# Kernel tuning notes

Hardware: AMD Instinct MI355X
Metric: run time of the kernel (lower is better)

The kernel has to match this reference:

```python
import jax, jax.numpy as jnp
import numpy as np

EPS = 1e-8
NEG_INF = -9e15  # matches torch masked_fill value


def setup_inputs() -> dict:
    key = jax.random.key(0)
    k1, k2 = jax.random.split(key)
    B, D = 4096, 512
    p1 = jax.random.normal(k1, (B, D), dtype=jnp.float32)
    p2 = jax.random.normal(k2, (B, D), dtype=jnp.float32)
    return {"p1": p1, "p2": p2}


def reference(p1, p2):
    # NT-Xent / InfoNCE loss as in SimCLR_MODEL.contrastive_loss (temperature = 1).
    z = jnp.concatenate([p1, p2], axis=0)              # [N, D], N = 2B
    # cosine similarity == GEMM of L2-normalized rows (torch eps clamp = 1e-8)
    zn = z / jnp.maximum(jnp.linalg.norm(z, axis=-1, keepdims=True), EPS)
    sim = zn @ zn.T                                     # [N, N]
    N = sim.shape[0]
    idx = jnp.arange(N)
    sim = sim.at[idx, idx].set(NEG_INF)                 # mask self-similarity
    # positive pair of row i is row (i + N/2) mod N (eye rolled by N/2)
    pos = sim[idx, (idx + N // 2) % N]                  # [N]
    nll = -pos + jax.nn.logsumexp(sim, axis=-1)
    return jnp.mean(nll)
```

## Files before the change

### kernel.cpp

```cpp
#include <hip/hip_runtime.h>
#include <hip/hip_bf16.h>
#include <math.h>

#define N_TOT 8192
#define HALF_N 4096
#define D_DIM 512
#define BM 128
#define BK 64
#define NKIT (D_DIM / BK)
#define NTILES 2080

#define WAIT_VM4 0xF74
#define WAIT_VM0 0xF70

typedef float f32x4_t __attribute__((ext_vector_type(4)));
typedef long long i64x2 __attribute__((ext_vector_type(2)));

typedef __attribute__((address_space(1))) unsigned int g_u32;
typedef __attribute__((address_space(3))) unsigned int l_u32;

__global__ __launch_bounds__(256) void k_normalize(
    const float* __restrict__ p1, const float* __restrict__ p2,
    unsigned char* __restrict__ zf8, float* __restrict__ rowsum,
    float* __restrict__ out)
{
    const int w = threadIdx.x >> 6;
    const int lane = threadIdx.x & 63;
    const int row = blockIdx.x * 4 + w;

    if (threadIdx.x < 4) rowsum[blockIdx.x * 4 + threadIdx.x] = 0.0f;
    if (blockIdx.x == 0 && threadIdx.x == 0) out[0] = 0.0f;

    const float* src = (row < HALF_N) ? p1 + (size_t)row * D_DIM
                                      : p2 + (size_t)(row - HALF_N) * D_DIM;
    float4 a = *(const float4*)(src + lane * 4);
    float4 b = *(const float4*)(src + 256 + lane * 4);
    float s = a.x*a.x + a.y*a.y + a.z*a.z + a.w*a.w
            + b.x*b.x + b.y*b.y + b.z*b.z + b.w*b.w;
    #pragma unroll
    for (int m = 1; m < 64; m <<= 1) s += __shfl_xor(s, m, 64);
    float inv = 1.0f / fmaxf(sqrtf(s), 1e-8f);

    int pk0 = __builtin_amdgcn_cvt_pk_fp8_f32(a.x * inv, a.y * inv, 0, false);
    pk0     = __builtin_amdgcn_cvt_pk_fp8_f32(a.z * inv, a.w * inv, pk0, true);
    int pk1 = __builtin_amdgcn_cvt_pk_fp8_f32(b.x * inv, b.y * inv, 0, false);
    pk1     = __builtin_amdgcn_cvt_pk_fp8_f32(b.z * inv, b.w * inv, pk1, true);

    unsigned char* dst = zf8 + (size_t)row * D_DIM;
    const int o0 = lane * 4;
    const int o1 = 256 + lane * 4;
    const int d0 = (o0 & ~63) + ((o0 >> 3) & 3) * 16 + ((o0 >> 5) & 1) * 8 + (o0 & 4);
    const int d1 = (o1 & ~63) + ((o1 >> 3) & 3) * 16 + ((o1 >> 5) & 1) * 8 + (o1 & 4);
    *(int*)(dst + d0) = pk0;
    *(int*)(dst + d1) = pk1;
}

__global__ __launch_bounds__(256, 4) void k_gemm(
    const unsigned char* __restrict__ zf8,
    float* __restrict__ rowsum, float* __restrict__ pos)
{
    __shared__ __align__(16) unsigned char As[3][BM * BK];
    __shared__ __align__(16) unsigned char Bs[3][BM * BK];

    const int tid = threadIdx.x;
    const int lane = tid & 63;
    const int w = tid >> 6;
    const int wr = w >> 1, wc = w & 1;
    const int q = lane >> 4, l15 = lane & 15;

    const int t = blockIdx.x;
    int bi = (int)((sqrtf(8.0f * (float)t + 1.0f) - 1.0f) * 0.5f);
    while ((bi + 1) * (bi + 2) / 2 <= t) ++bi;
    while (bi * (bi + 1) / 2 > t) --bi;
    const int bx = bi;
    const int by = t - bi * (bi + 1) / 2;
    const bool isDiag = (bx == by);
    const bool hasPos = (bx - by == 32);
    const int rowBase = by * BM;
    const int colBase = bx * BM;

    const int ci0 = tid;
    const int ci1 = 256 + tid;
    const int r0 = ci0 >> 2, cc0 = ci0 & 3;
    const int r1 = ci1 >> 2, cc1 = ci1 & 3;
    const int gc0 = cc0 ^ ((r0 >> 1) & 3);
    const int gc1 = cc1 ^ ((r1 >> 1) & 3);

    const unsigned char* gA0 = zf8 + (size_t)(rowBase + r0) * D_DIM + gc0 * 16;
    const unsigned char* gA1 = zf8 + (size_t)(rowBase + r1) * D_DIM + gc1 * 16;
    const unsigned char* gB0 = zf8 + (size_t)(colBase + r0) * D_DIM + gc0 * 16;
    const unsigned char* gB1 = zf8 + (size_t)(colBase + r1) * D_DIM + gc1 * 16;

    auto stage = [&](int buf, int kblk) {
        const int kb = kblk * BK;
        __builtin_amdgcn_global_load_lds((const g_u32*)(gA0 + kb), (l_u32*)&As[buf][ci0 * 16], 16, 0, 0);
        __builtin_amdgcn_global_load_lds((const g_u32*)(gA1 + kb), (l_u32*)&As[buf][ci1 * 16], 16, 0, 0);
        __builtin_amdgcn_global_load_lds((const g_u32*)(gB0 + kb), (l_u32*)&Bs[buf][ci0 * 16], 16, 0, 0);
        __builtin_amdgcn_global_load_lds((const g_u32*)(gB1 + kb), (l_u32*)&Bs[buf][ci1 * 16], 16, 0, 0);
    };

    f32x4_t acc[4][4] = {};

    stage(0, 0);
    stage(1, 1);

    #pragma unroll
    for (int it = 0; it < NKIT; it++) {
        const int cur = it % 3;
        if (it + 1 < NKIT) __builtin_amdgcn_s_waitcnt(WAIT_VM4);
        else               __builtin_amdgcn_s_waitcnt(WAIT_VM0);
        __builtin_amdgcn_s_barrier();

        if (it + 2 < NKIT) stage((it + 2) % 3, it + 2);

        i64x2 aF[4], bF[4];
        #pragma unroll
        for (int i = 0; i < 4; i++) {
            const int ra = wr * 64 + i * 16 + l15;
            const int rb = wc * 64 + i * 16 + l15;
            aF[i] = *(const i64x2*)&As[cur][ra * BK + (q ^ ((ra >> 1) & 3)) * 16];
            bF[i] = *(const i64x2*)&Bs[cur][rb * BK + (q ^ ((rb >> 1) & 3)) * 16];
        }
        #pragma unroll
        for (int h = 0; h < 2; h++)
            #pragma unroll
            for (int i = 0; i < 4; i++)
                #pragma unroll
                for (int j = 0; j < 4; j++)
                    acc[i][j] = __builtin_amdgcn_mfma_f32_16x16x32_fp8_fp8(
                        aF[i][h], bF[j][h], acc[i][j], 0, 0, 0);
    }

    float colacc[4] = {0.f, 0.f, 0.f, 0.f};
    #pragma unroll
    for (int i = 0; i < 4; i++) {
        #pragma unroll
        for (int r = 0; r < 4; r++) {
            const int row = rowBase + wr * 64 + i * 16 + q * 4 + r;
            float rs = 0.0f;
            #pragma unroll
            for (int j = 0; j < 4; j++) {
                const int col = colBase + wc * 64 + j * 16 + l15;
                const float c = acc[i][j][r];
                float e = __expf(c);
                if (isDiag && col == row) e = 0.0f;
                rs += e;
                colacc[j] += e;
                if (hasPos && col == row + HALF_N) { pos[row] = c; pos[col] = c; }
            }
            rs += __shfl_xor(rs, 1); rs += __shfl_xor(rs, 2);
            rs += __shfl_xor(rs, 4); rs += __shfl_xor(rs, 8);
            if (l15 == 0) atomicAdd(&rowsum[row], rs);
        }
    }
    if (!isDiag) {
        #pragma unroll
        for (int j = 0; j < 4; j++) {
            float cs = colacc[j];
            cs += __shfl_xor(cs, 16);
            cs += __shfl_xor(cs, 32);
            if (q == 0) atomicAdd(&rowsum[colBase + wc * 64 + j * 16 + l15], cs);
        }
    }
}

__global__ __launch_bounds__(256) void k_finalize(
    const float* __restrict__ rowsum, const float* __restrict__ pos,
    float* __restrict__ out)
{
    const int t = threadIdx.x;
    const int i = blockIdx.x * 256 + t;
    float s = logf(rowsum[i]) - pos[i];
    #pragma unroll
    for (int m = 1; m < 64; m <<= 1) s += __shfl_xor(s, m, 64);
    __shared__ float red[4];
    if ((t & 63) == 0) red[t >> 6] = s;
    __syncthreads();
    if (t == 0)
        atomicAdd(out, (red[0] + red[1] + red[2] + red[3]) * (1.0f / (float)N_TOT));
}

extern "C" void kernel_launch(void* const* d_in, const int* in_sizes, int n_in,
                              void* d_out, int out_size, void* d_ws, size_t ws_size,
                              hipStream_t stream) {
    const float* p1 = (const float*)d_in[0];
    const float* p2 = (const float*)d_in[1];

    unsigned char* zf8 = (unsigned char*)d_ws;
    float* rowsum = (float*)((char*)d_ws + (size_t)N_TOT * D_DIM);
    float* pos    = rowsum + N_TOT;
    float* outp   = (float*)d_out;

    k_normalize<<<N_TOT / 4, 256, 0, stream>>>(p1, p2, zf8, rowsum, outp);
    k_gemm<<<NTILES, 256, 0, stream>>>(zf8, rowsum, pos);
    k_finalize<<<N_TOT / 256, 256, 0, stream>>>(rowsum, pos, outp);
}
```

Baseline: 104.6 us.

## Enlarge GEMM tiles to 256x256 with 8 waves and double buffering

Raises the block tile from 128 to 256 rows and columns, uses 512 threads (8 waves in a 2x4 layout, each computing 128x64), and cuts the triangular tile count from 2080 to 528. The 3-stage waitcnt-based pipeline becomes a 2-stage double buffer synchronised with __syncthreads, and block indices are remapped so consecutive blocks are spread across the triangle. The aim is more data reuse per loaded byte and fewer atomics per tile. In exchange, 528 blocks may fill the GPU poorly, accumulator register pressure doubles, and the simpler pipeline overlaps memory with compute less.

After: 284.4 us. 172% more time.

```diff
diff --git a/kernel.cpp b/kernel.cpp
--- a/kernel.cpp
+++ b/kernel.cpp
@@ -5,13 +5,11 @@
 #define N_TOT 8192
 #define HALF_N 4096
 #define D_DIM 512
-#define BM 128
+#define BM 256
 #define BK 64
 #define NKIT (D_DIM / BK)
-#define NTILES 2080
-
-#define WAIT_VM4 0xF74
-#define WAIT_VM0 0xF70
+#define NTILES 528
+#define THREADS 512
 
 typedef float f32x4_t __attribute__((ext_vector_type(4)));
 typedef long long i64x2 __attribute__((ext_vector_type(2)));
@@ -55,32 +53,34 @@
     *(int*)(dst + d1) = pk1;
 }
 
-__global__ __launch_bounds__(256, 4) void k_gemm(
+__global__ __launch_bounds__(THREADS, 4) void k_gemm(
     const unsigned char* __restrict__ zf8,
     float* __restrict__ rowsum, float* __restrict__ pos)
 {
-    __shared__ __align__(16) unsigned char As[3][BM * BK];
-    __shared__ __align__(16) unsigned char Bs[3][BM * BK];
+    __shared__ __align__(16) unsigned char As[2][BM * BK];
+    __shared__ __align__(16) unsigned char Bs[2][BM * BK];
 
     const int tid = threadIdx.x;
     const int lane = tid & 63;
     const int w = tid >> 6;
-    const int wr = w >> 1, wc = w & 1;
+    const int wr = w >> 2, wc = w & 3;
     const int q = lane >> 4, l15 = lane & 15;
 
-    const int t = blockIdx.x;
+    const int t0 = blockIdx.x;
+    const int t = (t0 & 7) * (NTILES / 8) + (t0 >> 3);
+
     int bi = (int)((sqrtf(8.0f * (float)t + 1.0f) - 1.0f) * 0.5f);
     while ((bi + 1) * (bi + 2) / 2 <= t) ++bi;
     while (bi * (bi + 1) / 2 > t) --bi;
     const int bx = bi;
     const int by = t - bi * (bi + 1) / 2;
     const bool isDiag = (bx == by);
-    const bool hasPos = (bx - by == 32);
+    const bool hasPos = (bx - by == (HALF_N / BM));
     const int rowBase = by * BM;
     const int colBase = bx * BM;
 
     const int ci0 = tid;
-    const int ci1 = 256 + tid;
+    const int ci1 = tid + THREADS;
     const int r0 = ci0 >> 2, cc0 = ci0 & 3;
     const int r1 = ci1 >> 2, cc1 = ci1 & 3;
     const int gc0 = cc0 ^ ((r0 >> 1) & 3);
@@ -99,32 +99,31 @@
         __builtin_amdgcn_global_load_lds((const g_u32*)(gB1 + kb), (l_u32*)&Bs[buf][ci1 * 16], 16, 0, 0);
     };
 
-    f32x4_t acc[4][4] = {};
+    f32x4_t acc[8][4] = {};
 
     stage(0, 0);
-    stage(1, 1);
 
     #pragma unroll
     for (int it = 0; it < NKIT; it++) {
-        const int cur = it % 3;
-        if (it + 1 < NKIT) __builtin_amdgcn_s_waitcnt(WAIT_VM4);
-        else               __builtin_amdgcn_s_waitcnt(WAIT_VM0);
-        __builtin_amdgcn_s_barrier();
+        const int cur = it & 1;
+        __syncthreads();
+        if (it + 1 < NKIT) stage(cur ^ 1, it + 1);
 
-        if (it + 2 < NKIT) stage((it + 2) % 3, it + 2);
-
-        i64x2 aF[4], bF[4];
+        i64x2 aF[8], bF[4];
         #pragma unroll
-        for (int i = 0; i < 4; i++) {
-            const int ra = wr * 64 + i * 16 + l15;
-            const int rb = wc * 64 + i * 16 + l15;
+        for (int i = 0; i < 8; i++) {
+            const int ra = wr * 128 + i * 16 + l15;
             aF[i] = *(const i64x2*)&As[cur][ra * BK + (q ^ ((ra >> 1) & 3)) * 16];
-            bF[i] = *(const i64x2*)&Bs[cur][rb * BK + (q ^ ((rb >> 1) & 3)) * 16];
+        }
+        #pragma unroll
+        for (int j = 0; j < 4; j++) {
+            const int rb = wc * 64 + j * 16 + l15;
+            bF[j] = *(const i64x2*)&Bs[cur][rb * BK + (q ^ ((rb >> 1) & 3)) * 16];
         }
         #pragma unroll
         for (int h = 0; h < 2; h++)
             #pragma unroll
-            for (int i = 0; i < 4; i++)
+            for (int i = 0; i < 8; i++)
                 #pragma unroll
                 for (int j = 0; j < 4; j++)
                     acc[i][j] = __builtin_amdgcn_mfma_f32_16x16x32_fp8_fp8(
@@ -133,10 +132,10 @@
 
     float colacc[4] = {0.f, 0.f, 0.f, 0.f};
     #pragma unroll
-    for (int i = 0; i < 4; i++) {
+    for (int i = 0; i < 8; i++) {
         #pragma unroll
         for (int r = 0; r < 4; r++) {
-            const int row = rowBase + wr * 64 + i * 16 + q * 4 + r;
+            const int row = rowBase + wr * 128 + i * 16 + q * 4 + r;
             float rs = 0.0f;
             #pragma unroll
             for (int j = 0; j < 4; j++) {
@@ -192,6 +191,6 @@
     float* outp   = (float*)d_out;
 
     k_normalize<<<N_TOT / 4, 256, 0, stream>>>(p1, p2, zf8, rowsum, outp);
-    k_gemm<<<NTILES, 256, 0, stream>>>(zf8, rowsum, pos);
+    k_gemm<<<NTILES, THREADS, 0, stream>>>(zf8, rowsum, pos);
     k_finalize<<<N_TOT / 256, 256, 0, stream>>>(rowsum, pos, outp);
 }
```
